# Kernel optimization log

Measured on AMD Instinct MI355X. Metric: run time of the kernel, lower is better.

## Reference

```python
import jax, jax.numpy as jnp
import numpy as np

L, B, T, N, M = 2, 32, 256, 1024, 1024  # layers, batch, time, input feat, hidden


def setup_inputs() -> dict:
    key = jax.random.key(0)
    ks = jax.random.split(key, 7)
    s = 0.02  # weight init scale
    return {
        "x": jax.random.normal(ks[0], (B, T, N), dtype=jnp.float32),
        "h": jax.random.normal(ks[1], (L, B, M), dtype=jnp.float32) * 0.1,
        "c": jax.random.normal(ks[2], (L, B, M), dtype=jnp.float32) * 0.1,
        "Wih": jax.random.normal(ks[3], (L, 4 * M, N), dtype=jnp.float32) * s,
        "Whh": jax.random.normal(ks[4], (L, 4 * M, M), dtype=jnp.float32) * s,
        "bih": jnp.zeros((L, 4 * M), dtype=jnp.float32),
        "bhh": jnp.zeros((L, 4 * M), dtype=jnp.float32),
    }


def _lstm_cell(x_t, h_t, c_t, Wih_l, Whh_l, b_l):
    # gates: [i | f | g | o], matching torch.nn.LSTMCell layout
    gates = x_t @ Wih_l.T + h_t @ Whh_l.T + b_l  # (B, 4M)
    i, f, g, o = jnp.split(gates, 4, axis=-1)
    i, f, o = jax.nn.sigmoid(i), jax.nn.sigmoid(f), jax.nn.sigmoid(o)
    c_new = f * c_t + i * jnp.tanh(g)
    h_new = o * jnp.tanh(c_new)
    return h_new, c_new


def reference(x, h, c, Wih, Whh, bih, bhh):
    b_sum = bih + bhh  # (L, 4M)

    def step(carry, x_t):
        h_cur, c_cur = carry  # each (L, B, M)
        hs, cs = [], []
        inp = x_t
        for l in range(L):  # small fixed layer loop
            h_l, c_l = _lstm_cell(inp, h_cur[l], c_cur[l], Wih[l], Whh[l], b_sum[l])
            hs.append(h_l)
            cs.append(c_l)
            inp = h_l
        return (jnp.stack(hs, 0), jnp.stack(cs, 0)), inp  # emit top-layer h

    (h_final, c_final), outs_tbm = jax.lax.scan(step, (h, c), jnp.swapaxes(x, 0, 1))
    outs = jnp.swapaxes(outs_tbm, 0, 1)  # (B, T, M)
    return outs, h_final, c_final
```

## Files before the change

### kernel.cpp

```cpp
#include <hip/hip_runtime.h>


typedef __bf16 bf16x8 __attribute__((ext_vector_type(8)));
typedef float  f32x4  __attribute__((ext_vector_type(4)));
typedef unsigned u32x4 __attribute__((ext_vector_type(4)));

__device__ __forceinline__ unsigned short f2bf(float f) {
    union { float f; unsigned u; } v; v.f = f;
    unsigned u = v.u;
    unsigned r = u + 0x7fffu + ((u >> 16) & 1u);
    return (unsigned short)(r >> 16);
}
__device__ __forceinline__ float sigmoidf_fast(float x) {
    return 1.0f / (1.0f + __expf(-x));
}
__device__ __forceinline__ float tanhf_fast(float x) {
    return 1.0f - 2.0f / (__expf(2.0f * x) + 1.0f);
}

__global__ void cvt_w_concat(const float* __restrict__ src,
                             unsigned short* __restrict__ dst, int off, int n4) {
    int i = blockIdx.x * blockDim.x + threadIdx.x;
    int stride = gridDim.x * blockDim.x;
    for (; i < n4; i += stride) {
        float4 v = ((const float4*)src)[i];
        ushort4 o;
        o.x = f2bf(v.x); o.y = f2bf(v.y); o.z = f2bf(v.z); o.w = f2bf(v.w);
        int row = i >> 8;
        int c4  = i & 255;
        *(ushort4*)&dst[(size_t)row * 2048 + off + c4 * 4] = o;
    }
}

__global__ void cvt_x_tiles(const float* __restrict__ x,
                            unsigned short* __restrict__ xT) {
    int t = blockIdx.x, tid = threadIdx.x;
    unsigned short* tile = xT + (size_t)t * 32768;
    for (int b = 0; b < 32; ++b) {
        float4 v = *(const float4*)&x[((size_t)b * 256 + t) * 1024 + tid * 4];
        ushort4 o;
        o.x = f2bf(v.x); o.y = f2bf(v.y); o.z = f2bf(v.z); o.w = f2bf(v.w);
        *(ushort4*)&tile[(tid >> 2) * 512 + b * 16 + (tid & 3) * 4] = o;
    }
}

__global__ void cvt_h0_tiles(const float* __restrict__ h0,
                             unsigned short* __restrict__ h0T) {
    int l = blockIdx.x, tid = threadIdx.x;
    unsigned short* tile = h0T + (size_t)l * 32768;
    for (int b = 0; b < 32; ++b) {
        float4 v = *(const float4*)&h0[((size_t)l * 32 + b) * 1024 + tid * 4];
        ushort4 o;
        o.x = f2bf(v.x); o.y = f2bf(v.y); o.z = f2bf(v.z); o.w = f2bf(v.w);
        *(ushort4*)&tile[(tid >> 2) * 512 + b * 16 + (tid & 3) * 4] = o;
    }
}

__global__ void out_transpose(const float* __restrict__ outT,
                              float* __restrict__ out) {
    int t = blockIdx.x, tid = threadIdx.x;
    const float* tile = outT + (size_t)t * 32768;
    for (int b = 0; b < 32; ++b) {
        float4 v = *(const float4*)&tile[(tid >> 2) * 512 + b * 16 + (tid & 3) * 4];
        *(float4*)&out[((size_t)b * 256 + t) * 1024 + tid * 4] = v;
    }
}

__device__ __forceinline__ void pollge(const unsigned* fp, unsigned tgt) {
    while (true) {
        unsigned v = __hip_atomic_load(fp, __ATOMIC_RELAXED,
                                       __HIP_MEMORY_SCOPE_AGENT);
        if (__all((int)(v >= tgt))) break;
        __builtin_amdgcn_s_sleep(1);
    }
}

__global__ __launch_bounds__(256, 1) void lstm_fused(
    const unsigned short* __restrict__ Wcat,
    const unsigned short* __restrict__ xT,
    unsigned short* __restrict__ seqT,
    const unsigned short* __restrict__ h0T,
    unsigned short* __restrict__ hparT,
    float* __restrict__ outT,
    const float* __restrict__ c0,
    const float* __restrict__ bih, const float* __restrict__ bhh,
    float* __restrict__ out, unsigned int* flags)
{
    __shared__ __align__(16) unsigned short bufH[32][1024];
    __shared__ __align__(16) unsigned short bufX[32][1024];
    __shared__ __align__(16) unsigned short hout_bf[32][16];
    __shared__ __align__(16) float hout_f[32][16];

    const int tid  = threadIdx.x;
    const int lane = tid & 63;
    const int w    = tid >> 6;
    const int l    = blockIdx.x >> 6;
    const int bidl = blockIdx.x & 63;
    const int m0   = bidl * 16;
    const int n    = lane & 15;
    const int g    = lane >> 4;
    const int lk   = g * 8;
    const int nn7  = n & 7;

    char* const bH = (char*)&bufH[0][0];
    char* const bX = (char*)&bufX[0][0];
    float (*gred)[2][4][16][20] = (float (*)[2][4][16][20])bX;

    bf16x8 wx[32], wh[32];
    const unsigned short* Wl = Wcat + (size_t)l * 4096 * 2048;
    #pragma unroll
    for (int ct = 0; ct < 4; ct++) {
        int vc = ct * 16 + n;
        size_t jrow = (size_t)((vc & 3) * 1024 + m0 + (vc >> 2));
        #pragma unroll
        for (int kc = 0; kc < 8; kc++) {
            wx[ct*8+kc] = *(const bf16x8*)&Wl[jrow*2048 +        w*256 + kc*32 + lk];
            wh[ct*8+kc] = *(const bf16x8*)&Wl[jrow*2048 + 1024 + w*256 + kc*32 + lk];
        }
    }

    const int eb = lane >> 1;
    const int q  = lane & 1;
    const int em = m0 + 4 * w + 2 * q;
    float bs0[4], bs1[4];
    #pragma unroll
    for (int gg = 0; gg < 4; gg++) {
        bs0[gg] = bih[l*4096 + gg*1024 + em]     + bhh[l*4096 + gg*1024 + em];
        bs1[gg] = bih[l*4096 + gg*1024 + em + 1] + bhh[l*4096 + gg*1024 + em + 1];
    }
    float2 creg = *(const float2*)&c0[(size_t)l * 32768 + eb * 1024 + em];
    float2 hlast = {0.f, 0.f};
    const int uh = eb >> 4, urow = eb & 15;

    const int sb     = lane >> 1;
    const int halfk  = lane & 1;
    const int srcOff = w * 16384 + sb * 32 + halfk * 16;
    const int sbRow  = sb * 2048;
    const int ldsCol = w * 512 + halfk * 16;
    const int swz    = (sb & 7) << 4;

    const int hb64 = (nn7 >> 2) * 64;
    const int gx16 = (g ^ (nn7 & 3)) * 16;
    const int rOffA0 = n * 2048 + w * 512 + gx16 + hb64;
    const int rOffA1 = n * 2048 + w * 512 + gx16 + (64 - hb64);

    f32x4 acc0[4] = {}, acc1[4] = {};
    u32x4 hv[16];

    auto issue = [&](const char* tb, bool byp) {
        const char* gp = tb + srcOff;
        if (byp) {
            #pragma unroll
            for (int si = 0; si < 16; si++)
                asm volatile("global_load_dwordx4 %0, %1, off sc0 sc1"
                             : "=v"(hv[si]) : "v"(gp + si * 1024) : "memory");
        } else {
            #pragma unroll
            for (int si = 0; si < 16; si++)
                asm volatile("global_load_dwordx4 %0, %1, off"
                             : "=v"(hv[si]) : "v"(gp + si * 1024) : "memory");
        }
    };

    auto gemmbuf = [&](const char* base, const bf16x8* wfv) {
        const char* pA0 = base + rOffA0;
        const char* pA1 = base + rOffA1;
        const char* pB0 = pA0 + 16 * 2048;
        const char* pB1 = pA1 + 16 * 2048;
        #pragma unroll
        for (int kc2 = 0; kc2 < 4; kc2++) {
            bf16x8 a0 = *(const bf16x8*)(pA0 + kc2 * 128);
            bf16x8 a1 = *(const bf16x8*)(pB0 + kc2 * 128);
            #pragma unroll
            for (int ct = 0; ct < 4; ct++) {
                acc0[ct] = __builtin_amdgcn_mfma_f32_16x16x32_bf16(a0, wfv[ct*8+2*kc2],   acc0[ct],0,0,0);
                acc1[ct] = __builtin_amdgcn_mfma_f32_16x16x32_bf16(a1, wfv[ct*8+2*kc2],   acc1[ct],0,0,0);
            }
            bf16x8 b0 = *(const bf16x8*)(pA1 + kc2 * 128);
            bf16x8 b1 = *(const bf16x8*)(pB1 + kc2 * 128);
            #pragma unroll
            for (int ct = 0; ct < 4; ct++) {
                acc0[ct] = __builtin_amdgcn_mfma_f32_16x16x32_bf16(b0, wfv[ct*8+2*kc2+1], acc0[ct],0,0,0);
                acc1[ct] = __builtin_amdgcn_mfma_f32_16x16x32_bf16(b1, wfv[ct*8+2*kc2+1], acc1[ct],0,0,0);
            }
        }
    };

    auto stage_gemm_h = [&](const char* tb) {
        const char* gp = tb + srcOff;
        #pragma unroll
        for (int si = 0; si < 16; si++)
            asm volatile("global_load_dwordx4 %0, %1, off sc0 sc1"
                         : "=v"(hv[si]) : "v"(gp + si * 1024) : "memory");
        const char* pA0 = bH + rOffA0;
        const char* pA1 = bH + rOffA1;
        const char* pB0 = pA0 + 16 * 2048;
        const char* pB1 = pA1 + 16 * 2048;
#define SGRP(G4, VM) \
        asm volatile("s_waitcnt vmcnt(" VM ")" ::: "memory"); \
        _Pragma("unroll") \
        for (int si = 4*(G4); si < 4*(G4)+4; si++) \
            *(u32x4*)(bH + sbRow + ((ldsCol + si*32) ^ swz)) = hv[si]; \
        { \
            bf16x8 a0 = *(const bf16x8*)(pA0 + (G4)*128); \
            bf16x8 a1 = *(const bf16x8*)(pB0 + (G4)*128); \
            _Pragma("unroll") \
            for (int ct = 0; ct < 4; ct++) { \
                acc0[ct] = __builtin_amdgcn_mfma_f32_16x16x32_bf16(a0, wh[ct*8+2*(G4)],   acc0[ct],0,0,0); \
                acc1[ct] = __builtin_amdgcn_mfma_f32_16x16x32_bf16(a1, wh[ct*8+2*(G4)],   acc1[ct],0,0,0); \
            } \
            bf16x8 b0 = *(const bf16x8*)(pA1 + (G4)*128); \
            bf16x8 b1 = *(const bf16x8*)(pB1 + (G4)*128); \
            _Pragma("unroll") \
            for (int ct = 0; ct < 4; ct++) { \
                acc0[ct] = __builtin_amdgcn_mfma_f32_16x16x32_bf16(b0, wh[ct*8+2*(G4)+1], acc0[ct],0,0,0); \
                acc1[ct] = __builtin_amdgcn_mfma_f32_16x16x32_bf16(b1, wh[ct*8+2*(G4)+1], acc1[ct],0,0,0); \
            } \
        }
        SGRP(0, "12") SGRP(1, "8") SGRP(2, "4") SGRP(3, "0")
#undef SGRP
    };

    if (l == 0) {
        issue((const char*)xT, false);
        asm volatile("s_waitcnt vmcnt(0)" ::: "memory");
        #pragma unroll
        for (int si = 0; si < 16; si++)
            *(u32x4*)(bX + sbRow + ((ldsCol + si * 32) ^ swz)) = hv[si];
        gemmbuf(bX, wx);
    }
    __syncthreads();

    const int lag = l * 2;
    #pragma unroll 1
    for (int s = 0; s < 258; s++) {
        const int  t    = s - lag;
        const bool act  = (t >= 0) && (t < 256);
        const int  tn   = t + 1;
        const bool xact = (tn >= ((l == 0) ? 1 : 0)) && (tn <= 255);
        const char* xsrc = (l == 0) ? (const char*)(xT   + (size_t)tn * 32768)
                                    : (const char*)(seqT + (size_t)tn * 32768);

        if (act) {
            const char* hb = (t == 0)
                ? (const char*)(h0T + (size_t)l * 32768)
                : (l == 0 ? (const char*)(seqT + (size_t)(t - 1) * 32768)
                          : (const char*)(hparT + (size_t)((t - 1) & 1) * 32768));
            stage_gemm_h(hb);

            if (xact && w != 0) issue(xsrc, l == 1);

            {
                int r0 = g * 4;
                #pragma unroll
                for (int ct = 0; ct < 4; ct++) {
                    *(f32x4*)&gred[w][0][ct][n][r0] = acc0[ct];
                    *(f32x4*)&gred[w][1][ct][n][r0] = acc1[ct];
                }
            }
            __syncthreads();
            float g8[8];
            #pragma unroll
            for (int j = 0; j < 8; j++) {
                g8[j] = (gred[0][uh][w][8*q+j][urow] + gred[1][uh][w][8*q+j][urow])
                      + (gred[2][uh][w][8*q+j][urow] + gred[3][uh][w][8*q+j][urow]);
            }
            float gi0 = g8[0] + bs0[0], gf0 = g8[1] + bs0[1];
            float gg0 = g8[2] + bs0[2], go0 = g8[3] + bs0[3];
            float gi1 = g8[4] + bs1[0], gf1 = g8[5] + bs1[1];
            float gg1 = g8[6] + bs1[2], go1 = g8[7] + bs1[3];

            float c0n = sigmoidf_fast(gf0) * creg.x + sigmoidf_fast(gi0) * tanhf_fast(gg0);
            float c1n = sigmoidf_fast(gf1) * creg.y + sigmoidf_fast(gi1) * tanhf_fast(gg1);
            float h0v = sigmoidf_fast(go0) * tanhf_fast(c0n);
            float h1v = sigmoidf_fast(go1) * tanhf_fast(c1n);
            creg.x = c0n; creg.y = c1n;
            hlast.x = h0v; hlast.y = h1v;

            unsigned hp = (unsigned)f2bf(h0v) | ((unsigned)f2bf(h1v) << 16);
            *(unsigned*)&hout_bf[eb][4*w + 2*q] = hp;
            if (l == 1) {
                float2 hv2 = {h0v, h1v};
                *(float2*)&hout_f[eb][4*w + 2*q] = hv2;
            }
            __syncthreads();
            if (tid < 64) {
                u32x4 v = *(const u32x4*)((const char*)&hout_bf[0][0] + tid * 16);
                const char* dp = (l == 0)
                    ? (const char*)(seqT  + (size_t)t * 32768)       + bidl * 1024 + tid * 16
                    : (const char*)(hparT + (size_t)(t & 1) * 32768) + bidl * 1024 + tid * 16;
                asm volatile("global_store_dwordx4 %0, %1, off sc0 sc1"
                             :: "v"(dp), "v"(v) : "memory");
                asm volatile("s_waitcnt vmcnt(0)" ::: "memory");
                if (tid == 0)
                    __hip_atomic_store(flags + l * 64 + bidl, (unsigned)(s + 1),
                                       __ATOMIC_RELAXED, __HIP_MEMORY_SCOPE_AGENT);
            } else if (l == 1 && tid < 192) {
                int u = tid - 64;
                f32x4 v = *(const f32x4*)((const char*)&hout_f[0][0] + u * 16);
                *(f32x4*)((char*)outT + (size_t)t * 131072 + bidl * 2048 + u * 16) = v;
            }
            if (xact && w == 0) issue(xsrc, l == 1);
        } else {
            if (tid == 0)
                __hip_atomic_store(flags + l * 64 + bidl, (unsigned)(s + 1),
                                   __ATOMIC_RELAXED, __HIP_MEMORY_SCOPE_AGENT);
            if (xact) issue(xsrc, l == 1);
        }

        if (xact) {
            asm volatile("s_waitcnt vmcnt(0)" ::: "memory");
            #pragma unroll
            for (int si = 0; si < 16; si++)
                *(u32x4*)(bX + sbRow + ((ldsCol + si * 32) ^ swz)) = hv[si];
            #pragma unroll
            for (int ct = 0; ct < 4; ct++) {
                acc0[ct] = (f32x4){0.f, 0.f, 0.f, 0.f};
                acc1[ct] = (f32x4){0.f, 0.f, 0.f, 0.f};
            }
            gemmbuf(bX, wx);
        }

        if (tid < (l ? 128 : 64)) pollge(flags + tid, (unsigned)(s + 1));
        __syncthreads();
    }

    float* hF = out + (size_t)8192 * 1024 + (size_t)l * 32768;
    float* cF = out + (size_t)8192 * 1024 + 65536 + (size_t)l * 32768;
    float2 hf2 = {hlast.x, hlast.y};
    *(float2*)&hF[eb * 1024 + em] = hf2;
    float2 cf2 = {creg.x, creg.y};
    *(float2*)&cF[eb * 1024 + em] = cf2;
}

extern "C" void kernel_launch(void* const* d_in, const int* in_sizes, int n_in,
                              void* d_out, int out_size, void* d_ws, size_t ws_size,
                              hipStream_t stream)
{
    const float* x   = (const float*)d_in[0];
    const float* h0  = (const float*)d_in[1];
    const float* c0  = (const float*)d_in[2];
    const float* Wih = (const float*)d_in[3];
    const float* Whh = (const float*)d_in[4];
    const float* bih = (const float*)d_in[5];
    const float* bhh = (const float*)d_in[6];
    float* out = (float*)d_out;

    char* p = (char*)d_ws;
    unsigned short* xT    = (unsigned short*)p; p += (size_t)256 * 32768 * 2;
    unsigned short* seqT  = (unsigned short*)p; p += (size_t)256 * 32768 * 2;
    unsigned short* Wcat  = (unsigned short*)p; p += (size_t)2 * 4096 * 2048 * 2;
    unsigned short* h0T   = (unsigned short*)p; p += (size_t)2 * 32768 * 2;
    unsigned short* hparT = (unsigned short*)p; p += (size_t)2 * 32768 * 2;
    float*          outT  = (float*)p;          p += (size_t)256 * 32768 * 4;
    unsigned int*   flags = (unsigned int*)p;   p += 4096;

    hipMemsetAsync(flags, 0, 4096, stream);
    cvt_w_concat<<<1024, 256, 0, stream>>>(Wih, Wcat, 0,    2 * 4096 * 256);
    cvt_w_concat<<<1024, 256, 0, stream>>>(Whh, Wcat, 1024, 2 * 4096 * 256);
    cvt_x_tiles<<<256, 256, 0, stream>>>(x, xT);
    cvt_h0_tiles<<<2, 256, 0, stream>>>(h0, h0T);

    lstm_fused<<<128, 256, 0, stream>>>(Wcat, xT, seqT, h0T, hparT, outT,
                                        c0, bih, bhh, out, flags);

    out_transpose<<<256, 256, 0, stream>>>(outT, out);
}
```

Baseline: 1.526 ms.

## Store h directly per thread and pipeline x staging with its GEMM

Each thread now writes its bf16 h pair and fp32 output straight to global memory, replacing the LDS gather and the single-wave dwordx4 stores that followed a barrier. The x-tile prefetch for the next step is issued by all waves right after the h GEMM rather than split around the epilogue, and the x GEMM now interleaves LDS writes with MFMAs in four waitcnt-staged groups instead of waiting on every load first. Polling is widened to 128 flags for both layers. The intent is to cut a barrier and serialized store work from the recurrent critical path and overlap the x load latency with compute. The cost is many small 4-byte stores per thread in place of coalesced 16-byte ones, plus extra polling.

```diff
diff --git a/kernel.cpp b/kernel.cpp
--- a/kernel.cpp
+++ b/kernel.cpp
@@ -88,8 +88,6 @@
 {
     __shared__ __align__(16) unsigned short bufH[32][1024];
     __shared__ __align__(16) unsigned short bufX[32][1024];
-    __shared__ __align__(16) unsigned short hout_bf[32][16];
-    __shared__ __align__(16) float hout_f[32][16];
 
     const int tid  = threadIdx.x;
     const int lane = tid & 63;
@@ -132,6 +130,9 @@
     float2 hlast = {0.f, 0.f};
     const int uh = eb >> 4, urow = eb & 15;
 
+    const int exOff = bidl * 1024 + eb * 32 + (4 * w + 2 * q) * 2;
+    const int outOff = bidl * 2048 + eb * 64 + (4 * w + 2 * q) * 4;
+
     const int sb     = lane >> 1;
     const int halfk  = lane & 1;
     const int srcOff = w * 16384 + sb * 32 + halfk * 16;
@@ -159,30 +160,6 @@
             for (int si = 0; si < 16; si++)
                 asm volatile("global_load_dwordx4 %0, %1, off"
                              : "=v"(hv[si]) : "v"(gp + si * 1024) : "memory");
-        }
-    };
-
-    auto gemmbuf = [&](const char* base, const bf16x8* wfv) {
-        const char* pA0 = base + rOffA0;
-        const char* pA1 = base + rOffA1;
-        const char* pB0 = pA0 + 16 * 2048;
-        const char* pB1 = pA1 + 16 * 2048;
-        #pragma unroll
-        for (int kc2 = 0; kc2 < 4; kc2++) {
-            bf16x8 a0 = *(const bf16x8*)(pA0 + kc2 * 128);
-            bf16x8 a1 = *(const bf16x8*)(pB0 + kc2 * 128);
-            #pragma unroll
-            for (int ct = 0; ct < 4; ct++) {
-                acc0[ct] = __builtin_amdgcn_mfma_f32_16x16x32_bf16(a0, wfv[ct*8+2*kc2],   acc0[ct],0,0,0);
-                acc1[ct] = __builtin_amdgcn_mfma_f32_16x16x32_bf16(a1, wfv[ct*8+2*kc2],   acc1[ct],0,0,0);
-            }
-            bf16x8 b0 = *(const bf16x8*)(pA1 + kc2 * 128);
-            bf16x8 b1 = *(const bf16x8*)(pB1 + kc2 * 128);
-            #pragma unroll
-            for (int ct = 0; ct < 4; ct++) {
-                acc0[ct] = __builtin_amdgcn_mfma_f32_16x16x32_bf16(b0, wfv[ct*8+2*kc2+1], acc0[ct],0,0,0);
-                acc1[ct] = __builtin_amdgcn_mfma_f32_16x16x32_bf16(b1, wfv[ct*8+2*kc2+1], acc1[ct],0,0,0);
-            }
         }
     };
 
@@ -227,7 +204,27 @@
         #pragma unroll
         for (int si = 0; si < 16; si++)
             *(u32x4*)(bX + sbRow + ((ldsCol + si * 32) ^ swz)) = hv[si];
-        gemmbuf(bX, wx);
+        const char* pA0 = bX + rOffA0;
+        const char* pA1 = bX + rOffA1;
+        const char* pB0 = pA0 + 16 * 2048;
+        const char* pB1 = pA1 + 16 * 2048;
+        #pragma unroll
+        for (int kc2 = 0; kc2 < 4; kc2++) {
+            bf16x8 a0 = *(const bf16x8*)(pA0 + kc2 * 128);
+            bf16x8 a1 = *(const bf16x8*)(pB0 + kc2 * 128);
+            #pragma unroll
+            for (int ct = 0; ct < 4; ct++) {
+                acc0[ct] = __builtin_amdgcn_mfma_f32_16x16x32_bf16(a0, wx[ct*8+2*kc2],   acc0[ct],0,0,0);
+                acc1[ct] = __builtin_amdgcn_mfma_f32_16x16x32_bf16(a1, wx[ct*8+2*kc2],   acc1[ct],0,0,0);
+            }
+            bf16x8 b0 = *(const bf16x8*)(pA1 + kc2 * 128);
+            bf16x8 b1 = *(const bf16x8*)(pB1 + kc2 * 128);
+            #pragma unroll
+            for (int ct = 0; ct < 4; ct++) {
+                acc0[ct] = __builtin_amdgcn_mfma_f32_16x16x32_bf16(b0, wx[ct*8+2*kc2+1], acc0[ct],0,0,0);
+                acc1[ct] = __builtin_amdgcn_mfma_f32_16x16x32_bf16(b1, wx[ct*8+2*kc2+1], acc1[ct],0,0,0);
+            }
+        }
     }
     __syncthreads();
 
@@ -248,7 +245,7 @@
                           : (const char*)(hparT + (size_t)((t - 1) & 1) * 32768));
             stage_gemm_h(hb);
 
-            if (xact && w != 0) issue(xsrc, l == 1);
+            if (xact) issue(xsrc, l == 1);
 
             {
                 int r0 = g * 4;
@@ -278,29 +275,22 @@
             hlast.x = h0v; hlast.y = h1v;
 
             unsigned hp = (unsigned)f2bf(h0v) | ((unsigned)f2bf(h1v) << 16);
-            *(unsigned*)&hout_bf[eb][4*w + 2*q] = hp;
-            if (l == 1) {
-                float2 hv2 = {h0v, h1v};
-                *(float2*)&hout_f[eb][4*w + 2*q] = hv2;
+            {
+                char* dp = (l == 0)
+                    ? (char*)(seqT  + (size_t)t * 32768)       + exOff
+                    : (char*)(hparT + (size_t)(t & 1) * 32768) + exOff;
+                asm volatile("global_store_dword %0, %1, off sc0 sc1"
+                             :: "v"(dp), "v"(hp) : "memory");
+                if (l == 1) {
+                    float2 hv2 = {h0v, h1v};
+                    *(float2*)((char*)outT + (size_t)t * 131072 + outOff) = hv2;
+                }
+                asm volatile("s_waitcnt vmcnt(0)" ::: "memory");
             }
             __syncthreads();
-            if (tid < 64) {
-                u32x4 v = *(const u32x4*)((const char*)&hout_bf[0][0] + tid * 16);
-                const char* dp = (l == 0)
-                    ? (const char*)(seqT  + (size_t)t * 32768)       + bidl * 1024 + tid * 16
-                    : (const char*)(hparT + (size_t)(t & 1) * 32768) + bidl * 1024 + tid * 16;
-                asm volatile("global_store_dwordx4 %0, %1, off sc0 sc1"
-                             :: "v"(dp), "v"(v) : "memory");
-                asm volatile("s_waitcnt vmcnt(0)" ::: "memory");
-                if (tid == 0)
-                    __hip_atomic_store(flags + l * 64 + bidl, (unsigned)(s + 1),
-                                       __ATOMIC_RELAXED, __HIP_MEMORY_SCOPE_AGENT);
-            } else if (l == 1 && tid < 192) {
-                int u = tid - 64;
-                f32x4 v = *(const f32x4*)((const char*)&hout_f[0][0] + u * 16);
-                *(f32x4*)((char*)outT + (size_t)t * 131072 + bidl * 2048 + u * 16) = v;
-            }
-            if (xact && w == 0) issue(xsrc, l == 1);
+            if (tid == 0)
+                __hip_atomic_store(flags + l * 64 + bidl, (unsigned)(s + 1),
+                                   __ATOMIC_RELAXED, __HIP_MEMORY_SCOPE_AGENT);
         } else {
             if (tid == 0)
                 __hip_atomic_store(flags + l * 64 + bidl, (unsigned)(s + 1),
@@ -309,19 +299,41 @@
         }
 
         if (xact) {
-            asm volatile("s_waitcnt vmcnt(0)" ::: "memory");
-            #pragma unroll
-            for (int si = 0; si < 16; si++)
-                *(u32x4*)(bX + sbRow + ((ldsCol + si * 32) ^ swz)) = hv[si];
             #pragma unroll
             for (int ct = 0; ct < 4; ct++) {
                 acc0[ct] = (f32x4){0.f, 0.f, 0.f, 0.f};
                 acc1[ct] = (f32x4){0.f, 0.f, 0.f, 0.f};
             }
-            gemmbuf(bX, wx);
-        }
-
-        if (tid < (l ? 128 : 64)) pollge(flags + tid, (unsigned)(s + 1));
+            const char* pA0 = bX + rOffA0;
+            const char* pA1 = bX + rOffA1;
+            const char* pB0 = pA0 + 16 * 2048;
+            const char* pB1 = pA1 + 16 * 2048;
+#define TGRP(G4, VM) \
+            asm volatile("s_waitcnt vmcnt(" VM ")" ::: "memory"); \
+            _Pragma("unroll") \
+            for (int si = 4*(G4); si < 4*(G4)+4; si++) \
+                *(u32x4*)(bX + sbRow + ((ldsCol + si*32) ^ swz)) = hv[si]; \
+            { \
+                bf16x8 a0 = *(const bf16x8*)(pA0 + (G4)*128); \
+                bf16x8 a1 = *(const bf16x8*)(pB0 + (G4)*128); \
+                _Pragma("unroll") \
+                for (int ct = 0; ct < 4; ct++) { \
+                    acc0[ct] = __builtin_amdgcn_mfma_f32_16x16x32_bf16(a0, wx[ct*8+2*(G4)],   acc0[ct],0,0,0); \
+                    acc1[ct] = __builtin_amdgcn_mfma_f32_16x16x32_bf16(a1, wx[ct*8+2*(G4)],   acc1[ct],0,0,0); \
+                } \
+                bf16x8 b0 = *(const bf16x8*)(pA1 + (G4)*128); \
+                bf16x8 b1 = *(const bf16x8*)(pB1 + (G4)*128); \
+                _Pragma("unroll") \
+                for (int ct = 0; ct < 4; ct++) { \
+                    acc0[ct] = __builtin_amdgcn_mfma_f32_16x16x32_bf16(b0, wx[ct*8+2*(G4)+1], acc0[ct],0,0,0); \
+                    acc1[ct] = __builtin_amdgcn_mfma_f32_16x16x32_bf16(b1, wx[ct*8+2*(G4)+1], acc1[ct],0,0,0); \
+                } \
+            }
+            TGRP(0, "12") TGRP(1, "8") TGRP(2, "4") TGRP(3, "0")
+#undef TGRP
+        }
+
+        if (tid < 128) pollge(flags + tid, (unsigned)(s + 1));
         __syncthreads();
     }
 
```

After: 1.335 ms. 1.14x faster.
